# Performance work log

Hardware: AMD Instinct MI355X
Metric: run time of the kernel (lower is better)

Reference implementation:

```python
import jax, jax.numpy as jnp
import numpy as np

N_CODES = 8
CODE_DIM = 256

def setup_inputs() -> dict:
    key = jax.random.key(0)
    k1, k2 = jax.random.split(key)
    z = jax.random.normal(k1, (8, 32768, CODE_DIM), dtype=jnp.float32)
    # embedding initialized uniform(-1/n_codes, 1/n_codes) like the torch module
    emb = jax.random.uniform(k2, (N_CODES, CODE_DIM), dtype=jnp.float32,
                             minval=-1.0 / N_CODES, maxval=1.0 / N_CODES)
    return {"z": z, "emb": emb}

def reference(z, emb):
    # squared euclidean distances: ||z||^2 + ||e||^2 - 2 z.e^T  -> [B, T, n_codes]
    d = (jnp.sum(z ** 2, axis=-1, keepdims=True)
         + jnp.sum(emb ** 2, axis=-1)
         - 2.0 * jnp.einsum('btd,nd->btn', z, emb))
    idx = jnp.argmin(d, axis=-1)            # [B, T] int
    z_q = emb[idx]                          # [B, T, code_dim]
    # straight-through estimator
    z_q = z + jax.lax.stop_gradient(z_q - z)
    return (z_q, idx)
```

## Files before the change

### kernel.cpp

```cpp
#include <hip/hip_runtime.h>


#define NC    8
#define DIM   256
#define TPW   32
#define WPB   2
#define THREADS (WPB * 64)
#define BATCH 8

typedef float f32x4 __attribute__((ext_vector_type(4)));

__global__ __launch_bounds__(THREADS, 2)
void vq_kernel(const float* __restrict__ z, const float* __restrict__ emb,
               float* __restrict__ zq, float* __restrict__ fidx)
{
    __shared__ float lds[WPB][2][BATCH * DIM];

    const int lane = threadIdx.x & 63;
    const int w    = threadIdx.x >> 6;
    const int wid  = blockIdx.x * WPB + w;

    const int c2 = lane & 1;
    const int b1 = (lane >> 1) & 1, b2 = (lane >> 2) & 1;
    const int b3 = (lane >> 3) & 1, b4 = (lane >> 4) & 1, b5 = (lane >> 5) & 1;
    const int kappa = 4 * c2 + 2 * b1 + b2;
    const int gidx  = lane & 7;
    const int tau   = 4 * b3 + 2 * b4 + b5;

    double e64[4][8];
#pragma unroll
    for (int m = 0; m < 4; ++m) {
        const int row = 4 * c2 + m;
        const float4 ea = *reinterpret_cast<const float4*>(emb + row * DIM + 4 * lane);
        const float4 eb = *reinterpret_cast<const float4*>(emb + row * DIM + 4 * (lane ^ 1));
        e64[m][0] = ea.x; e64[m][1] = ea.y; e64[m][2] = ea.z; e64[m][3] = ea.w;
        e64[m][4] = eb.x; e64[m][5] = eb.y; e64[m][6] = eb.z; e64[m][7] = eb.w;
    }

    double es[4];
#pragma unroll
    for (int m = 0; m < 4; ++m) {
        double s = 0.0;
#pragma unroll
        for (int j = 0; j < 8; ++j) s += e64[m][j] * e64[m][j];
        es[m] = s;
    }
    double est[2];
#pragma unroll
    for (int i = 0; i < 2; ++i) {
        double keep = b1 ? es[i + 2] : es[i];
        double send = b1 ? es[i]     : es[i + 2];
        est[i] = keep + __shfl_xor(send, 2, 64);
    }
    double esv = (b2 ? est[1] : est[0]) + __shfl_xor(b2 ? est[0] : est[1], 4, 64);
    esv += __shfl_xor(esv, 8, 64);
    esv += __shfl_xor(esv, 16, 64);
    esv += __shfl_xor(esv, 32, 64);
    const double esq_my = esv;

    const long long tok0 = (long long)wid * TPW;

    double val[8];

    auto STAGE = [&](int bufi, int bidx) {
        const float* s = z + (tok0 + (long long)bidx * BATCH) * DIM + 4 * lane;
        float* d = &lds[w][bufi][0];
#pragma unroll
        for (int t = 0; t < BATCH; ++t)
            __builtin_amdgcn_global_load_lds(
                (const unsigned int*)(s + (size_t)t * DIM),
                (unsigned int*)(d + t * DIM), 16, 0, 0);
    };

    auto COMPUTE = [&](int bufi) {
        const float* bb = &lds[w][bufi][0];
#pragma unroll
        for (int t = 0; t < BATCH; ++t) {
            const float4 cA = *reinterpret_cast<const float4*>(bb + t * DIM + 4 * lane);
            const float4 cB = *reinterpret_cast<const float4*>(bb + t * DIM + 4 * (lane ^ 1));
            double acc[4];
            {
                const double z0 = cA.x, z1 = cA.y, z2 = cA.z, z3 = cA.w;
#pragma unroll
                for (int m = 0; m < 4; ++m)
                    acc[m] = (z0 * e64[m][0] + z1 * e64[m][1])
                           + (z2 * e64[m][2] + z3 * e64[m][3]);
            }
            {
                const double z4 = cB.x, z5 = cB.y, z6 = cB.z, z7 = cB.w;
#pragma unroll
                for (int m = 0; m < 4; ++m)
                    acc[m] += (z4 * e64[m][4] + z5 * e64[m][5])
                            + (z6 * e64[m][6] + z7 * e64[m][7]);
            }
            double ft[2];
#pragma unroll
            for (int i = 0; i < 2; ++i) {
                double keep = b1 ? acc[i + 2] : acc[i];
                double send = b1 ? acc[i]     : acc[i + 2];
                ft[i] = keep + __shfl_xor(send, 2, 64);
            }
            val[t] = (b2 ? ft[1] : ft[0]) + __shfl_xor(b2 ? ft[0] : ft[1], 4, 64);
        }
    };

    auto TAIL = [&](int bidx) {
        double tt[4];
#pragma unroll
        for (int i = 0; i < 4; ++i) {
            double keep = b3 ? val[i + 4] : val[i];
            double send = b3 ? val[i]     : val[i + 4];
            tt[i] = keep + __shfl_xor(send, 8, 64);
        }
        double uu[2];
#pragma unroll
        for (int i = 0; i < 2; ++i) {
            double keep = b4 ? tt[i + 2] : tt[i];
            double send = b4 ? tt[i]     : tt[i + 2];
            uu[i] = keep + __shfl_xor(send, 16, 64);
        }
        const double dot = (b5 ? uu[1] : uu[0]) + __shfl_xor(b5 ? uu[0] : uu[1], 32, 64);

        const double dist = esq_my - 2.0 * dot;

        unsigned long long u = (unsigned long long)__double_as_longlong(dist);
        u = (u >> 63) ? ~u : (u | 0x8000000000000000ULL);
        unsigned long long key = (u & ~7ULL) | (unsigned long long)kappa;
#pragma unroll
        for (int m = 1; m <= 4; m <<= 1) {
            unsigned long long ok = __shfl_xor(key, m, 64);
            key = (ok < key) ? ok : key;
        }
        const int widx = (int)(key & 7ULL);

        const long long row = tok0 + (long long)bidx * BATCH + tau;
        float* qrow = zq + row * DIM;
        const float* erow = emb + widx * DIM;
#pragma unroll
        for (int j = 0; j < 8; ++j) {
            const int ch = gidx + 8 * j;
            const f32x4 q = *reinterpret_cast<const f32x4*>(erow + 4 * ch);
            __builtin_nontemporal_store(q, reinterpret_cast<f32x4*>(qrow + 4 * ch));
        }
        if (gidx == 0) fidx[row] = (float)widx;
    };

    STAGE(0, 0);
    STAGE(1, 1);

    asm volatile("s_waitcnt vmcnt(8)" ::: "memory");
    __builtin_amdgcn_sched_barrier(0);
    COMPUTE(0); TAIL(0);
    STAGE(0, 2);

    asm volatile("s_waitcnt vmcnt(17)" ::: "memory");
    __builtin_amdgcn_sched_barrier(0);
    COMPUTE(1); TAIL(1);
    STAGE(1, 3);

    asm volatile("s_waitcnt vmcnt(17)" ::: "memory");
    __builtin_amdgcn_sched_barrier(0);
    COMPUTE(0); TAIL(2);

    asm volatile("s_waitcnt vmcnt(9)" ::: "memory");
    __builtin_amdgcn_sched_barrier(0);
    COMPUTE(1); TAIL(3);
}

extern "C" void kernel_launch(void* const* d_in, const int* in_sizes, int n_in,
                              void* d_out, int out_size, void* d_ws, size_t ws_size,
                              hipStream_t stream)
{
    const float* z   = (const float*)d_in[0];
    const float* emb = (const float*)d_in[1];
    float* out = (float*)d_out;

    const long long ntok = (long long)in_sizes[0] / DIM;
    float* zq   = out;
    float* fidx = out + (size_t)ntok * DIM;

    const int blocks = (int)(ntok / (TPW * WPB));

    vq_kernel<<<blocks, THREADS, 0, stream>>>(z, emb, zq, fidx);
}
```

Before: 95.08 us.

## Halve pipeline batch, store embeddings as float, raise occupancy to five waves

Shrinks the per-stage token batch from 8 to 4, which halves the LDS footprint and the val register array. The pipeline deepens from 4 to 8 stages, with waitcnt values adjusted to match. Embeddings are kept in float registers and converted to double when used, and launch bounds rise from 2 to 5 blocks per CU to increase occupancy for this memory-bound kernel. The cross-lane reduction is reorganised so the lane-32 halves split the output row store, which adds more wait/compute phases and per-use conversions in exchange.

```diff
diff --git a/kernel.cpp b/kernel.cpp
--- a/kernel.cpp
+++ b/kernel.cpp
@@ -6,11 +6,16 @@
 #define TPW   32
 #define WPB   2
 #define THREADS (WPB * 64)
-#define BATCH 8
+#define BATCH 4
 
 typedef float f32x4 __attribute__((ext_vector_type(4)));
 
-__global__ __launch_bounds__(THREADS, 2)
+#define WAITV(n) do { \
+    asm volatile("s_waitcnt vmcnt(" #n ")" ::: "memory"); \
+    __builtin_amdgcn_sched_barrier(0); \
+} while (0)
+
+__global__ __launch_bounds__(THREADS, 5)
 void vq_kernel(const float* __restrict__ z, const float* __restrict__ emb,
                float* __restrict__ zq, float* __restrict__ fidx)
 {
@@ -25,16 +30,16 @@
     const int b3 = (lane >> 3) & 1, b4 = (lane >> 4) & 1, b5 = (lane >> 5) & 1;
     const int kappa = 4 * c2 + 2 * b1 + b2;
     const int gidx  = lane & 7;
-    const int tau   = 4 * b3 + 2 * b4 + b5;
+    const int tau   = 2 * b3 + b4;
 
-    double e64[4][8];
+    float e32[4][8];
 #pragma unroll
     for (int m = 0; m < 4; ++m) {
         const int row = 4 * c2 + m;
         const float4 ea = *reinterpret_cast<const float4*>(emb + row * DIM + 4 * lane);
         const float4 eb = *reinterpret_cast<const float4*>(emb + row * DIM + 4 * (lane ^ 1));
-        e64[m][0] = ea.x; e64[m][1] = ea.y; e64[m][2] = ea.z; e64[m][3] = ea.w;
-        e64[m][4] = eb.x; e64[m][5] = eb.y; e64[m][6] = eb.z; e64[m][7] = eb.w;
+        e32[m][0] = ea.x; e32[m][1] = ea.y; e32[m][2] = ea.z; e32[m][3] = ea.w;
+        e32[m][4] = eb.x; e32[m][5] = eb.y; e32[m][6] = eb.z; e32[m][7] = eb.w;
     }
 
     double es[4];
@@ -42,7 +47,10 @@
     for (int m = 0; m < 4; ++m) {
         double s = 0.0;
 #pragma unroll
-        for (int j = 0; j < 8; ++j) s += e64[m][j] * e64[m][j];
+        for (int j = 0; j < 8; ++j) {
+            const double e = (double)e32[m][j];
+            s += e * e;
+        }
         es[m] = s;
     }
     double est[2];
@@ -60,7 +68,7 @@
 
     const long long tok0 = (long long)wid * TPW;
 
-    double val[8];
+    double val[BATCH];
 
     auto STAGE = [&](int bufi, int bidx) {
         const float* s = z + (tok0 + (long long)bidx * BATCH) * DIM + 4 * lane;
@@ -83,15 +91,15 @@
                 const double z0 = cA.x, z1 = cA.y, z2 = cA.z, z3 = cA.w;
 #pragma unroll
                 for (int m = 0; m < 4; ++m)
-                    acc[m] = (z0 * e64[m][0] + z1 * e64[m][1])
-                           + (z2 * e64[m][2] + z3 * e64[m][3]);
+                    acc[m] = (z0 * (double)e32[m][0] + z1 * (double)e32[m][1])
+                           + (z2 * (double)e32[m][2] + z3 * (double)e32[m][3]);
             }
             {
                 const double z4 = cB.x, z5 = cB.y, z6 = cB.z, z7 = cB.w;
 #pragma unroll
                 for (int m = 0; m < 4; ++m)
-                    acc[m] += (z4 * e64[m][4] + z5 * e64[m][5])
-                            + (z6 * e64[m][6] + z7 * e64[m][7]);
+                    acc[m] += (z4 * (double)e32[m][4] + z5 * (double)e32[m][5])
+                            + (z6 * (double)e32[m][6] + z7 * (double)e32[m][7]);
             }
             double ft[2];
 #pragma unroll
@@ -100,26 +108,20 @@
                 double send = b1 ? acc[i]     : acc[i + 2];
                 ft[i] = keep + __shfl_xor(send, 2, 64);
             }
-            val[t] = (b2 ? ft[1] : ft[0]) + __shfl_xor(b2 ? ft[0] : ft[1], 4, 64);
+            double v = (b2 ? ft[1] : ft[0]) + __shfl_xor(b2 ? ft[0] : ft[1], 4, 64);
+            val[t] = v + __shfl_xor(v, 32, 64);
         }
     };
 
     auto TAIL = [&](int bidx) {
-        double tt[4];
+        double tt[2];
 #pragma unroll
-        for (int i = 0; i < 4; ++i) {
-            double keep = b3 ? val[i + 4] : val[i];
-            double send = b3 ? val[i]     : val[i + 4];
+        for (int i = 0; i < 2; ++i) {
+            double keep = b3 ? val[i + 2] : val[i];
+            double send = b3 ? val[i]     : val[i + 2];
             tt[i] = keep + __shfl_xor(send, 8, 64);
         }
-        double uu[2];
-#pragma unroll
-        for (int i = 0; i < 2; ++i) {
-            double keep = b4 ? tt[i + 2] : tt[i];
-            double send = b4 ? tt[i]     : tt[i + 2];
-            uu[i] = keep + __shfl_xor(send, 16, 64);
-        }
-        const double dot = (b5 ? uu[1] : uu[0]) + __shfl_xor(b5 ? uu[0] : uu[1], 32, 64);
+        const double dot = (b4 ? tt[1] : tt[0]) + __shfl_xor(b4 ? tt[0] : tt[1], 16, 64);
 
         const double dist = esq_my - 2.0 * dot;
 
@@ -137,34 +139,24 @@
         float* qrow = zq + row * DIM;
         const float* erow = emb + widx * DIM;
 #pragma unroll
-        for (int j = 0; j < 8; ++j) {
-            const int ch = gidx + 8 * j;
+        for (int j = 0; j < 4; ++j) {
+            const int ch = gidx + 8 * b5 + 16 * j;
             const f32x4 q = *reinterpret_cast<const f32x4*>(erow + 4 * ch);
             __builtin_nontemporal_store(q, reinterpret_cast<f32x4*>(qrow + 4 * ch));
         }
-        if (gidx == 0) fidx[row] = (float)widx;
+        if (gidx == 0 && b5 == 0) fidx[row] = (float)widx;
     };
 
-    STAGE(0, 0);
-    STAGE(1, 1);
+    STAGE(0, 0); STAGE(1, 1);
 
-    asm volatile("s_waitcnt vmcnt(8)" ::: "memory");
-    __builtin_amdgcn_sched_barrier(0);
-    COMPUTE(0); TAIL(0);
-    STAGE(0, 2);
-
-    asm volatile("s_waitcnt vmcnt(17)" ::: "memory");
-    __builtin_amdgcn_sched_barrier(0);
-    COMPUTE(1); TAIL(1);
-    STAGE(1, 3);
-
-    asm volatile("s_waitcnt vmcnt(17)" ::: "memory");
-    __builtin_amdgcn_sched_barrier(0);
-    COMPUTE(0); TAIL(2);
-
-    asm volatile("s_waitcnt vmcnt(9)" ::: "memory");
-    __builtin_amdgcn_sched_barrier(0);
-    COMPUTE(1); TAIL(3);
+    WAITV(4); COMPUTE(0); TAIL(0); STAGE(0, 2);
+    WAITV(9); COMPUTE(1); TAIL(1); STAGE(1, 3);
+    WAITV(9); COMPUTE(0); TAIL(2); STAGE(0, 4);
+    WAITV(9); COMPUTE(1); TAIL(3); STAGE(1, 5);
+    WAITV(9); COMPUTE(0); TAIL(4); STAGE(0, 6);
+    WAITV(9); COMPUTE(1); TAIL(5); STAGE(1, 7);
+    WAITV(9); COMPUTE(0); TAIL(6);
+    WAITV(5); COMPUTE(1); TAIL(7);
 }
 
 extern "C" void kernel_launch(void* const* d_in, const int* in_sizes, int n_in,
```

Result: slower. 312.2 us (+228.3%).
